# Kernel tuning notes

Measured on AMD Instinct MI355X. Metric: run time of the kernel, lower is better.

The kernel has to match this reference:

```python
import jax, jax.numpy as jnp
import numpy as np
import math

B, N, D, H = 2, 64, 256, 8
DK = D // H


def setup_inputs() -> dict:
    key = jax.random.key(0)
    ks = jax.random.split(key, 12)
    s = 1.0 / math.sqrt(D)
    inp = {
        "state": jax.random.normal(ks[0], (B, N, N, D), dtype=jnp.float32),
        "mask": jnp.zeros((B, N, N, N), dtype=bool),
        "W_lk": jax.random.normal(ks[1], (D, D), dtype=jnp.float32) * s,
        "b_lk": jnp.zeros((D,), dtype=jnp.float32),
        "W_rk": jax.random.normal(ks[2], (D, D), dtype=jnp.float32) * s,
        "b_rk": jnp.zeros((D,), dtype=jnp.float32),
        "W_lv": jax.random.normal(ks[3], (D, D), dtype=jnp.float32) * s,
        "b_lv": jnp.zeros((D,), dtype=jnp.float32),
        "W_rv": jax.random.normal(ks[4], (D, D), dtype=jnp.float32) * s,
        "b_rv": jnp.zeros((D,), dtype=jnp.float32),
        "W_o": jax.random.normal(ks[5], (D, D), dtype=jnp.float32) * s,
        "b_o": jnp.zeros((D,), dtype=jnp.float32),
    }
    return inp


def _proj(x, W, b):
    # torch nn.Linear: x @ W.T + b, then view to heads
    y = jnp.einsum('bxyd,ed->bxye', x, W) + b
    return y.reshape(B, N, N, H, DK)


def reference(state, mask, W_lk, b_lk, W_rk, b_rk, W_lv, b_lv, W_rv, b_rv, W_o, b_o):
    left_k = _proj(state, W_lk, b_lk)   # [B,N,N,H,DK]
    right_k = _proj(state, W_rk, b_rk)
    left_v = _proj(state, W_lv, b_lv)
    right_v = _proj(state, W_rv, b_rv)

    # triangle-style scores over node triples (x, a, y): [B,N,N,N,H]
    scores = jnp.einsum('bxahd,bayhd->bxayh', left_k, right_k) / math.sqrt(DK)
    scores = jnp.where(mask[..., None], jnp.float32(-1000.0), scores)
    att = jax.nn.softmax(scores, axis=2)  # softmax over intermediate node a

    # val[b,x,a,y,h,d] = left_v[b,x,a,h,d] * right_v[b,a,y,h,d] (materialized as in torch)
    val = jnp.einsum('bxahd,bayhd->bxayhd', left_v, right_v)
    x = jnp.einsum('bxayh,bxayhd->bxyhd', att, val)  # sum over a
    x = x.reshape(B, N, N, D)
    return jnp.einsum('bxyd,ed->bxye', x, W_o) + b_o
```

## Files before the change

### kernel.cpp

```cpp
#include <hip/hip_runtime.h>

#define B 2
#define N 64
#define D 256
#define H 8
#define DK 32
#define M (B * N * N)

typedef __attribute__((ext_vector_type(8))) short bf16x8;
typedef __attribute__((ext_vector_type(4))) float f32x4;
typedef __attribute__((ext_vector_type(2))) float f32x2;

#define PROJ_ELEMS (2097152)

__device__ __forceinline__ ushort f2b(float f) {
    union { float f; unsigned u; } v; v.f = f;
    unsigned r = v.u + 0x7fffu + ((v.u >> 16) & 1u);
    return (ushort)(r >> 16);
}
__device__ __forceinline__ float b2f(ushort u) {
    union { unsigned u; float f; } v; v.u = ((unsigned)u) << 16; return v.f;
}
__device__ __forceinline__ f32x2 up2(unsigned u) {
    union { unsigned u; float f; } lo, hi;
    lo.u = u << 16; hi.u = u & 0xffff0000u;
    f32x2 r; r.x = lo.f; r.y = hi.f; return r;
}

__device__ __forceinline__ void glds16(const ushort* g, ushort* l) {
    __builtin_amdgcn_global_load_lds(
        (const __attribute__((address_space(1))) unsigned int*)g,
        (__attribute__((address_space(3))) unsigned int*)l, 16, 0, 0);
}

__global__ __launch_bounds__(256) void cast_all(const float* __restrict__ state,
                                                const float* __restrict__ W_lk, const float* __restrict__ W_rk,
                                                const float* __restrict__ W_lv, const float* __restrict__ W_rv,
                                                const float* __restrict__ W_o,
                                                const float* __restrict__ b_lk, const float* __restrict__ b_rk,
                                                const float* __restrict__ b_lv, const float* __restrict__ b_rv,
                                                const float* __restrict__ b_o,
                                                ushort* __restrict__ state_bf,
                                                ushort* __restrict__ Wcat,
                                                float* __restrict__ bias_cat) {
    const int gid = blockIdx.x * 256 + threadIdx.x;
    const float* Ws[5] = {W_lk, W_rk, W_lv, W_rv, W_o};
    const float* bs[5] = {b_lk, b_rk, b_lv, b_rv, b_o};

    if (gid < 1280) bias_cat[gid] = bs[gid >> 8][gid & 255];

    if (gid < 524288) {
        float4 v = *(const float4*)&state[(size_t)gid * 4];
        ushort4 o = {f2b(v.x), f2b(v.y), f2b(v.z), f2b(v.w)};
        *(ushort4*)&state_bf[(size_t)gid * 4] = o;
    } else {
        int u = gid - 524288;
        int row = u >> 6;
        int k4 = (u & 63) * 4;
        const float* W = Ws[row >> 8];
        float4 v = *(const float4*)&W[(size_t)(row & 255) * 256 + k4];
        ushort4 o = {f2b(v.x), f2b(v.y), f2b(v.z), f2b(v.w)};
        *(ushort4*)&Wcat[(size_t)row * 256 + k4] = o;
    }
}

template <int BF16OUT, int RELAYOUT>
__global__ __launch_bounds__(256) void gemm_mfma(const ushort* __restrict__ A,
                                                 const ushort* __restrict__ Bw,
                                                 const float* __restrict__ bias,
                                                 void* __restrict__ Cv, int ldc) {
    __shared__ __align__(16) ushort As[128 * 32];
    __shared__ __align__(16) ushort Bs[128 * 32];
    const int tid = threadIdx.x;
    const int lane = tid & 63;
    const int wave = tid >> 6;
    const int wm = (wave & 1) * 64;
    const int wn = (wave >> 1) * 64;
    const int row0 = blockIdx.x * 128;
    const int col0 = blockIdx.y * 128;

    const int lr = lane >> 2;
    const int lkq = (lane & 3) * 8;

    const ushort* gA0 = A + (size_t)(row0 + wave * 32 + lr) * 256 + lkq;
    const ushort* gA1 = gA0 + 16 * 256;
    const ushort* gB0 = Bw + (size_t)(col0 + wave * 32 + lr) * 256 + lkq;
    const ushort* gB1 = gB0 + 16 * 256;
    ushort* lA0 = &As[(wave * 32) * 32];
    ushort* lA1 = &As[(wave * 32 + 16) * 32];
    ushort* lB0 = &Bs[(wave * 32) * 32];
    ushort* lB1 = &Bs[(wave * 32 + 16) * 32];

    const int fr = lane & 15;
    const int fk = (lane >> 4) * 8;

    f32x4 acc[4][4] = {};

    for (int k0 = 0; k0 < 256; k0 += 32) {
        __syncthreads();
        glds16(gA0 + k0, lA0);
        glds16(gA1 + k0, lA1);
        glds16(gB0 + k0, lB0);
        glds16(gB1 + k0, lB1);
        __syncthreads();

        bf16x8 af[4], bf[4];
#pragma unroll
        for (int i = 0; i < 4; ++i)
            af[i] = *(const bf16x8*)&As[(wm + i * 16 + fr) * 32 + fk];
#pragma unroll
        for (int j = 0; j < 4; ++j)
            bf[j] = *(const bf16x8*)&Bs[(wn + j * 16 + fr) * 32 + fk];
#pragma unroll
        for (int i = 0; i < 4; ++i)
#pragma unroll
            for (int j = 0; j < 4; ++j)
                acc[i][j] = __builtin_amdgcn_mfma_f32_16x16x32_bf16(af[i], bf[j], acc[i][j], 0, 0, 0);
    }

#pragma unroll
    for (int j = 0; j < 4; ++j) {
        const int col = col0 + wn + j * 16 + (lane & 15);
        const float bv = bias[col];
#pragma unroll
        for (int i = 0; i < 4; ++i) {
            const int rbase = row0 + wm + i * 16 + (lane >> 4) * 4;
#pragma unroll
            for (int r = 0; r < 4; ++r) {
                float o = acc[i][j][r] + bv;
                if (RELAYOUT) {
                    const int row = rbase + r;
                    const int bb = row >> 12, rr = row & 4095;
                    const int proj = col >> 8, hh = (col >> 5) & 7, dk = col & 31;
                    ((ushort*)Cv)[(size_t)proj * PROJ_ELEMS +
                                  ((size_t)(bb * 8 + hh) * 4096 + rr) * 32 + dk] = f2b(o);
                } else if (BF16OUT) {
                    ((ushort*)Cv)[(size_t)(rbase + r) * ldc + col] = f2b(o);
                } else {
                    ((float*)Cv)[(size_t)(rbase + r) * ldc + col] = o;
                }
            }
        }
    }
}

__global__ __launch_bounds__(512, 4) void fused_attn(const ushort* __restrict__ P,
                                                     const unsigned char* __restrict__ mask,
                                                     ushort* __restrict__ xbuf) {
    __shared__ __align__(16) ushort LVb[16 * 512];
    __shared__ __align__(16) ushort RVb[16 * 512];
    __shared__ __align__(16) float atts[16 * 16 * 20];
    __shared__ float mstate[16 * 20];
    __shared__ float lstate[16 * 20];
    __shared__ float alphas[16 * 20];

    const int bh = blockIdx.z;
    const int b = bh >> 3, h = bh & 7;
    const int x0 = blockIdx.x * 16, y0 = blockIdx.y * 16;
    const int tid = threadIdx.x;
    const int lane = tid & 63, wave = tid >> 6;

    const size_t HB = (size_t)bh * 4096 * 32;
    const ushort* PLK = P + HB;
    const ushort* PRK = P + (size_t)1 * PROJ_ELEMS + HB;
    const ushort* PLV = P + (size_t)2 * PROJ_ELEMS + HB;
    const ushort* PRV = P + (size_t)3 * PROJ_ELEMS + HB;

    const int y2 = (tid >> 4) & 3, dp = tid & 15;
    const int sx = tid >> 4, sy = tid & 15;
    if (tid < 256) {
        mstate[sx * 20 + sy] = -3.0e38f;
        lstate[sx * 20 + sy] = 0.0f;
    }

    f32x2 acc[2][4] = {};
    const float scale = 0.17677669529663687f;

    const int pg = lane ^ (((lane >> 4) & 1) | (((lane >> 5) & 1) << 2));
    int ru[4];
#pragma unroll
    for (int j = 0; j < 4; ++j)
        ru[j] = (((y2 * 4 + j) * 16 + dp) ^ ((y2 & 1) << 2) ^ ((y2 & 2) << 3));

    for (int ac = 0; ac < N; ac += 16) {
        __syncthreads();
        {
            const int r2 = wave * 2;
            glds16(PLV + ((size_t)(x0 + r2) * 64 + ac) * 32 + lane * 8, &LVb[r2 * 512]);
            glds16(PLV + ((size_t)(x0 + r2 + 1) * 64 + ac) * 32 + lane * 8, &LVb[(r2 + 1) * 512]);
            glds16(PRV + ((size_t)(ac + r2) * 64 + y0) * 32 + pg * 8, &RVb[r2 * 512]);
            glds16(PRV + ((size_t)(ac + r2 + 1) * 64 + y0) * 32 + pg * 8, &RVb[(r2 + 1) * 512]);
        }
        {
            const int fr = lane & 15, fk = (lane >> 4) * 8;
            const int yq = lane & 15, xq = (lane >> 4) * 4;
#pragma unroll
            for (int aw = 0; aw < 2; ++aw) {
                const int a = wave * 2 + aw;
                bf16x8 af = *(const bf16x8*)&PLK[((size_t)(x0 + fr) * 64 + ac + a) * 32 + fk];
                bf16x8 bf = *(const bf16x8*)&PRK[((size_t)(ac + a) * 64 + y0 + fr) * 32 + fk];
                f32x4 s = {};
                s = __builtin_amdgcn_mfma_f32_16x16x32_bf16(af, bf, s, 0, 0, 0);
#pragma unroll
                for (int rr = 0; rr < 4; ++rr) {
                    const int x = xq + rr;
                    float sv = s[rr] * scale;
                    if (mask[((size_t)(b * N + x0 + x) * N + ac + a) * N + y0 + yq]) sv = -1000.0f;
                    atts[(a * 16 + x) * 20 + yq] = sv;
                }
            }
        }
        __syncthreads();

        if (tid < 256) {
            float mc = -3.0e38f;
#pragma unroll
            for (int a = 0; a < 16; ++a) mc = fmaxf(mc, atts[(a * 16 + sx) * 20 + sy]);
            const float mold = mstate[sx * 20 + sy];
            const float mnew = fmaxf(mold, mc);
            const float alpha = __expf(mold - mnew);
            float ps = 0.0f;
#pragma unroll
            for (int a = 0; a < 16; ++a) {
                float p = __expf(atts[(a * 16 + sx) * 20 + sy] - mnew);
                atts[(a * 16 + sx) * 20 + sy] = p;
                ps += p;
            }
            lstate[sx * 20 + sy] = lstate[sx * 20 + sy] * alpha + ps;
            mstate[sx * 20 + sy] = mnew;
            alphas[sx * 20 + sy] = alpha;
        }
        __syncthreads();

#pragma unroll
        for (int i = 0; i < 2; ++i) {
            const int x = wave * 2 + i;
            float4 av = *(const float4*)&alphas[x * 20 + y2 * 4];
            const float* ap = (const float*)&av;
#pragma unroll
            for (int j = 0; j < 4; ++j) acc[i][j] *= ap[j];
        }
        {
            const unsigned* LV32 = (const unsigned*)LVb;
            const unsigned* RV32 = (const unsigned*)RVb;
#pragma unroll
            for (int a = 0; a < 16; ++a) {
                f32x2 lv0 = up2(LV32[((wave * 2) * 16 + a) * 16 + dp]);
                f32x2 lv1 = up2(LV32[((wave * 2 + 1) * 16 + a) * 16 + dp]);
                f32x2 rv[4];
#pragma unroll
                for (int j = 0; j < 4; ++j) rv[j] = up2(RV32[a * 256 + ru[j]]);
                float4 wv0 = *(const float4*)&atts[(a * 16 + wave * 2) * 20 + y2 * 4];
                float4 wv1 = *(const float4*)&atts[(a * 16 + wave * 2 + 1) * 20 + y2 * 4];
                const float* w0 = (const float*)&wv0;
                const float* w1 = (const float*)&wv1;
#pragma unroll
                for (int j = 0; j < 4; ++j) {
                    acc[0][j] += (lv0 * w0[j]) * rv[j];
                    acc[1][j] += (lv1 * w1[j]) * rv[j];
                }
            }
        }
    }

#pragma unroll
    for (int i = 0; i < 2; ++i) {
        const int x = wave * 2 + i;
        float4 lq = *(const float4*)&lstate[x * 20 + y2 * 4];
        const float* lp = (const float*)&lq;
#pragma unroll
        for (int j = 0; j < 4; ++j) {
            const float il = 1.0f / lp[j];
            ushort2 o = {f2b(acc[i][j].x * il), f2b(acc[i][j].y * il)};
            *(ushort2*)&xbuf[(((size_t)b * N + x0 + x) * N + y0 + y2 * 4 + j) * D + h * DK + 2 * dp] = o;
        }
    }
}

extern "C" void kernel_launch(void* const* d_in, const int* in_sizes, int n_in,
                              void* d_out, int out_size, void* d_ws, size_t ws_size,
                              hipStream_t stream) {
    const float* state = (const float*)d_in[0];
    const unsigned char* mask = (const unsigned char*)d_in[1];
    const float* W_lk = (const float*)d_in[2];
    const float* b_lk = (const float*)d_in[3];
    const float* W_rk = (const float*)d_in[4];
    const float* b_rk = (const float*)d_in[5];
    const float* W_lv = (const float*)d_in[6];
    const float* b_lv = (const float*)d_in[7];
    const float* W_rv = (const float*)d_in[8];
    const float* b_rv = (const float*)d_in[9];
    const float* W_o = (const float*)d_in[10];
    const float* b_o = (const float*)d_in[11];
    float* out = (float*)d_out;

    char* ws = (char*)d_ws;
    ushort* P_bf = (ushort*)ws;
    ws += (size_t)4 * PROJ_ELEMS * 2;
    float* bias_cat = (float*)ws;
    ws += 1280 * 4;
    ushort* state_bf = (ushort*)ws;
    ws += (size_t)M * D * 2;
    ushort* Wcat = (ushort*)ws;
    ws += (size_t)1280 * 256 * 2;
    ushort* xbuf_bf = (ushort*)ws;

    cast_all<<<2368, 256, 0, stream>>>(state, W_lk, W_rk, W_lv, W_rv, W_o,
                                       b_lk, b_rk, b_lv, b_rv, b_o,
                                       state_bf, Wcat, bias_cat);
    gemm_mfma<1, 1><<<dim3(M / 128, 8), 256, 0, stream>>>(state_bf, Wcat, bias_cat, P_bf, 1024);
    fused_attn<<<dim3(4, 4, B * H), 512, 0, stream>>>(P_bf, mask, xbuf_bf);
    gemm_mfma<0, 0><<<dim3(M / 128, 2), 256, 0, stream>>>(xbuf_bf, Wcat + 1024 * 256, bias_cat + 1024, out, 256);
}
```

Before: 123.6 us.

## Double-buffer attention V staging, remap thread-to-output layout, batch GEMM K loads

The attention kernel now double-buffers the left and right value tiles in shared memory, so the loads for the next 16-wide chunk of the intermediate node are issued while the current chunk is accumulated. Each thread now owns one y and eight contiguous head dimensions, which allows 128-bit shared reads and a single 128-bit store of the bf16 output. The projection GEMM stages four K-slices at a time, cutting the barriers per tile from 16 to 4. The costs are more shared memory in both kernels and a lower occupancy hint for the attention kernel (launch bounds 512,4 to 512,2).

```diff
diff --git a/kernel.cpp b/kernel.cpp
--- a/kernel.cpp
+++ b/kernel.cpp
@@ -69,8 +69,8 @@
                                                  const ushort* __restrict__ Bw,
                                                  const float* __restrict__ bias,
                                                  void* __restrict__ Cv, int ldc) {
-    __shared__ __align__(16) ushort As[128 * 32];
-    __shared__ __align__(16) ushort Bs[128 * 32];
+    __shared__ __align__(16) ushort As[4][128 * 32];
+    __shared__ __align__(16) ushort Bs[4][128 * 32];
     const int tid = threadIdx.x;
     const int lane = tid & 63;
     const int wave = tid >> 6;
@@ -86,36 +86,39 @@
     const ushort* gA1 = gA0 + 16 * 256;
     const ushort* gB0 = Bw + (size_t)(col0 + wave * 32 + lr) * 256 + lkq;
     const ushort* gB1 = gB0 + 16 * 256;
-    ushort* lA0 = &As[(wave * 32) * 32];
-    ushort* lA1 = &As[(wave * 32 + 16) * 32];
-    ushort* lB0 = &Bs[(wave * 32) * 32];
-    ushort* lB1 = &Bs[(wave * 32 + 16) * 32];
 
     const int fr = lane & 15;
     const int fk = (lane >> 4) * 8;
 
     f32x4 acc[4][4] = {};
 
-    for (int k0 = 0; k0 < 256; k0 += 32) {
-        __syncthreads();
-        glds16(gA0 + k0, lA0);
-        glds16(gA1 + k0, lA1);
-        glds16(gB0 + k0, lB0);
-        glds16(gB1 + k0, lB1);
-        __syncthreads();
-
-        bf16x8 af[4], bf[4];
-#pragma unroll
-        for (int i = 0; i < 4; ++i)
-            af[i] = *(const bf16x8*)&As[(wm + i * 16 + fr) * 32 + fk];
-#pragma unroll
-        for (int j = 0; j < 4; ++j)
-            bf[j] = *(const bf16x8*)&Bs[(wn + j * 16 + fr) * 32 + fk];
-#pragma unroll
-        for (int i = 0; i < 4; ++i)
+    for (int half = 0; half < 2; ++half) {
+        const int k0 = half * 128;
+        __syncthreads();
+#pragma unroll
+        for (int pp = 0; pp < 4; ++pp) {
+            glds16(gA0 + k0 + pp * 32, &As[pp][(wave * 32) * 32]);
+            glds16(gA1 + k0 + pp * 32, &As[pp][(wave * 32 + 16) * 32]);
+            glds16(gB0 + k0 + pp * 32, &Bs[pp][(wave * 32) * 32]);
+            glds16(gB1 + k0 + pp * 32, &Bs[pp][(wave * 32 + 16) * 32]);
+        }
+        __syncthreads();
+
+#pragma unroll
+        for (int pp = 0; pp < 4; ++pp) {
+            bf16x8 af[4], bf[4];
+#pragma unroll
+            for (int i = 0; i < 4; ++i)
+                af[i] = *(const bf16x8*)&As[pp][(wm + i * 16 + fr) * 32 + fk];
 #pragma unroll
             for (int j = 0; j < 4; ++j)
-                acc[i][j] = __builtin_amdgcn_mfma_f32_16x16x32_bf16(af[i], bf[j], acc[i][j], 0, 0, 0);
+                bf[j] = *(const bf16x8*)&Bs[pp][(wn + j * 16 + fr) * 32 + fk];
+#pragma unroll
+            for (int i = 0; i < 4; ++i)
+#pragma unroll
+                for (int j = 0; j < 4; ++j)
+                    acc[i][j] = __builtin_amdgcn_mfma_f32_16x16x32_bf16(af[i], bf[j], acc[i][j], 0, 0, 0);
+        }
     }
 
 #pragma unroll
@@ -144,11 +147,11 @@
     }
 }
 
-__global__ __launch_bounds__(512, 4) void fused_attn(const ushort* __restrict__ P,
+__global__ __launch_bounds__(512, 2) void fused_attn(const ushort* __restrict__ P,
                                                      const unsigned char* __restrict__ mask,
                                                      ushort* __restrict__ xbuf) {
-    __shared__ __align__(16) ushort LVb[16 * 512];
-    __shared__ __align__(16) ushort RVb[16 * 512];
+    __shared__ __align__(16) ushort LVb[2][16 * 512];
+    __shared__ __align__(16) ushort RVb[2][16 * 512];
     __shared__ __align__(16) float atts[16 * 16 * 20];
     __shared__ float mstate[16 * 20];
     __shared__ float lstate[16 * 20];
@@ -166,31 +169,39 @@
     const ushort* PLV = P + (size_t)2 * PROJ_ELEMS + HB;
     const ushort* PRV = P + (size_t)3 * PROJ_ELEMS + HB;
 
-    const int y2 = (tid >> 4) & 3, dp = tid & 15;
+    const int gy = lane >> 2;
+    const int du = lane & 3;
     const int sx = tid >> 4, sy = tid & 15;
     if (tid < 256) {
         mstate[sx * 20 + sy] = -3.0e38f;
         lstate[sx * 20 + sy] = 0.0f;
     }
 
+    const int sa = lane >> 2, soct = lane & 3;
+    const int r2 = wave * 2;
+
     f32x2 acc[2][4] = {};
     const float scale = 0.17677669529663687f;
 
-    const int pg = lane ^ (((lane >> 4) & 1) | (((lane >> 5) & 1) << 2));
-    int ru[4];
-#pragma unroll
-    for (int j = 0; j < 4; ++j)
-        ru[j] = (((y2 * 4 + j) * 16 + dp) ^ ((y2 & 1) << 2) ^ ((y2 & 2) << 3));
-
-    for (int ac = 0; ac < N; ac += 16) {
-        __syncthreads();
-        {
-            const int r2 = wave * 2;
-            glds16(PLV + ((size_t)(x0 + r2) * 64 + ac) * 32 + lane * 8, &LVb[r2 * 512]);
-            glds16(PLV + ((size_t)(x0 + r2 + 1) * 64 + ac) * 32 + lane * 8, &LVb[(r2 + 1) * 512]);
-            glds16(PRV + ((size_t)(ac + r2) * 64 + y0) * 32 + pg * 8, &RVb[r2 * 512]);
-            glds16(PRV + ((size_t)(ac + r2 + 1) * 64 + y0) * 32 + pg * 8, &RVb[(r2 + 1) * 512]);
-        }
+#define STAGE(ac_, buf_)                                                                     \
+    do {                                                                                     \
+        glds16(PLV + ((size_t)(x0 + r2) * 64 + (ac_) + sa) * 32 + soct * 8,                  \
+               &LVb[buf_][r2 * 512]);                                                        \
+        glds16(PLV + ((size_t)(x0 + r2 + 1) * 64 + (ac_) + sa) * 32 + soct * 8,              \
+               &LVb[buf_][(r2 + 1) * 512]);                                                  \
+        glds16(PRV + ((size_t)((ac_) + r2) * 64 + y0 + sa) * 32 + soct * 8,                  \
+               &RVb[buf_][r2 * 512]);                                                        \
+        glds16(PRV + ((size_t)((ac_) + r2 + 1) * 64 + y0 + sa) * 32 + soct * 8,              \
+               &RVb[buf_][(r2 + 1) * 512]);                                                  \
+    } while (0)
+
+    STAGE(0, 0);
+
+    for (int c = 0; c < 4; ++c) {
+        const int ac = c * 16;
+        const int cur = c & 1;
+        __syncthreads();
+
         {
             const int fr = lane & 15, fk = (lane >> 4) * 8;
             const int yq = lane & 15, xq = (lane >> 4) * 4;
@@ -232,32 +243,32 @@
         }
         __syncthreads();
 
+        if (c < 3) STAGE(ac + 16, cur ^ 1);
+
 #pragma unroll
         for (int i = 0; i < 2; ++i) {
-            const int x = wave * 2 + i;
-            float4 av = *(const float4*)&alphas[x * 20 + y2 * 4];
-            const float* ap = (const float*)&av;
-#pragma unroll
-            for (int j = 0; j < 4; ++j) acc[i][j] *= ap[j];
-        }
+            const float av = alphas[(wave * 2 + i) * 20 + gy];
+#pragma unroll
+            for (int q = 0; q < 4; ++q) acc[i][q] *= av;
+        }
+
         {
-            const unsigned* LV32 = (const unsigned*)LVb;
-            const unsigned* RV32 = (const unsigned*)RVb;
+            const unsigned* LV32 = (const unsigned*)&LVb[cur][0];
+            const unsigned* RV32 = (const unsigned*)&RVb[cur][0];
 #pragma unroll
             for (int a = 0; a < 16; ++a) {
-                f32x2 lv0 = up2(LV32[((wave * 2) * 16 + a) * 16 + dp]);
-                f32x2 lv1 = up2(LV32[((wave * 2 + 1) * 16 + a) * 16 + dp]);
-                f32x2 rv[4];
-#pragma unroll
-                for (int j = 0; j < 4; ++j) rv[j] = up2(RV32[a * 256 + ru[j]]);
-                float4 wv0 = *(const float4*)&atts[(a * 16 + wave * 2) * 20 + y2 * 4];
-                float4 wv1 = *(const float4*)&atts[(a * 16 + wave * 2 + 1) * 20 + y2 * 4];
-                const float* w0 = (const float*)&wv0;
-                const float* w1 = (const float*)&wv1;
-#pragma unroll
-                for (int j = 0; j < 4; ++j) {
-                    acc[0][j] += (lv0 * w0[j]) * rv[j];
-                    acc[1][j] += (lv1 * w1[j]) * rv[j];
+                const uint4 rvw = *(const uint4*)&RV32[a * 256 + gy * 16 + du * 4];
+                const f32x2 rv0 = up2(rvw.x), rv1 = up2(rvw.y);
+                const f32x2 rv2 = up2(rvw.z), rv3 = up2(rvw.w);
+#pragma unroll
+                for (int i = 0; i < 2; ++i) {
+                    const int x = wave * 2 + i;
+                    const uint4 lvw = *(const uint4*)&LV32[x * 256 + a * 16 + du * 4];
+                    const float w = atts[(a * 16 + x) * 20 + gy];
+                    acc[i][0] += (up2(lvw.x) * w) * rv0;
+                    acc[i][1] += (up2(lvw.y) * w) * rv1;
+                    acc[i][2] += (up2(lvw.z) * w) * rv2;
+                    acc[i][3] += (up2(lvw.w) * w) * rv3;
                 }
             }
         }
@@ -266,15 +277,17 @@
 #pragma unroll
     for (int i = 0; i < 2; ++i) {
         const int x = wave * 2 + i;
-        float4 lq = *(const float4*)&lstate[x * 20 + y2 * 4];
-        const float* lp = (const float*)&lq;
-#pragma unroll
-        for (int j = 0; j < 4; ++j) {
-            const float il = 1.0f / lp[j];
-            ushort2 o = {f2b(acc[i][j].x * il), f2b(acc[i][j].y * il)};
-            *(ushort2*)&xbuf[(((size_t)b * N + x0 + x) * N + y0 + y2 * 4 + j) * D + h * DK + 2 * dp] = o;
-        }
-    }
+        const float il = 1.0f / lstate[x * 20 + gy];
+        ushort o[8] __attribute__((aligned(16)));
+#pragma unroll
+        for (int q = 0; q < 4; ++q) {
+            o[2 * q]     = f2b(acc[i][q].x * il);
+            o[2 * q + 1] = f2b(acc[i][q].y * il);
+        }
+        *(uint4*)&xbuf[(((size_t)b * N + x0 + x) * N + y0 + gy) * D + h * DK + du * 8] =
+            *(const uint4*)o;
+    }
+#undef STAGE
 }
 
 extern "C" void kernel_launch(void* const* d_in, const int* in_sizes, int n_in,
```

Result: no change. 122.1 us (-1.3%).
